# Kernel tuning notes

Measured on AMD Instinct MI355X. Metric: run time of the kernel, lower is better.

The kernel has to match this reference:

```python
import jax, jax.numpy as jnp
import numpy as np

H = 32          # num_attention_heads
HD = 128        # head_dim
HID = H * HD    # hidden_size = 4096
KB_LEN = 1024   # number of KB entries
TOPK = 128      # top_k_kb (dynamic_sparsify=True)
ROPE_THETA = 10000.0
PAD = -1000000000.0  # PADDING_VALUE


def rope_cos_sin(position_ids, head_dim, theta):
    inv_freq = 1.0 / (theta ** (jnp.arange(0, head_dim, 2, dtype=jnp.float32) / head_dim))
    freqs = position_ids.astype(jnp.float32)[..., None] * inv_freq  # [B,q,hd/2]
    emb = jnp.concatenate([freqs, freqs], axis=-1)                  # [B,q,hd]
    return jnp.cos(emb), jnp.sin(emb)


def rotate_half(x):
    half = x.shape[-1] // 2
    return jnp.concatenate([-x[..., half:], x[..., :half]], axis=-1)


def apply_rope(q, k, cos, sin):
    cos = cos[:, None]  # [B,1,q,hd]
    sin = sin[:, None]
    return q * cos + rotate_half(q) * sin, k * cos + rotate_half(k) * sin


def setup_inputs() -> dict:
    key = jax.random.key(0)
    ks = jax.random.split(key, 9)
    B, Q = 1, 2048
    w_scale = 0.02  # keep activations numerically sane
    hidden_states = jax.random.normal(ks[0], (B, Q, HID), jnp.float32)
    causal = jnp.where(jnp.tril(jnp.ones((Q, Q), bool)), 0.0, PAD).astype(jnp.float32)
    attention_mask = jnp.broadcast_to(causal[None, None], (B, 1, Q, Q))
    position_ids = jnp.broadcast_to(jnp.arange(Q)[None], (B, Q))
    kb_keys = jax.random.normal(ks[1], (KB_LEN, HID), jnp.float32)
    kb_values = jax.random.normal(ks[2], (KB_LEN, HID), jnp.float32)
    Wq = jax.random.normal(ks[3], (HID, HID), jnp.float32) * w_scale
    Wq2 = jax.random.normal(ks[4], (HID, HID), jnp.float32) * w_scale
    Wk = jax.random.normal(ks[5], (HID, HID), jnp.float32) * w_scale
    Wv = jax.random.normal(ks[6], (HID, HID), jnp.float32) * w_scale
    Wo = jax.random.normal(ks[7], (HID, HID), jnp.float32) * w_scale
    score_shift = jnp.zeros((H, 1), jnp.float32) - 3.0
    return {"hidden_states": hidden_states, "attention_mask": attention_mask,
            "position_ids": position_ids, "kb_keys": kb_keys, "kb_values": kb_values,
            "Wq": Wq, "Wq2": Wq2, "Wk": Wk, "Wv": Wv, "Wo": Wo,
            "score_shift": score_shift}


def kblam_attention(hidden_states, attention_mask, position_ids, kb_keys, kb_values,
                    Wq, Wq2, Wk, Wv, Wo, score_shift):
    B, Q, _ = hidden_states.shape
    scale = 1.0 / np.sqrt(HD)

    def heads(x):  # [B,Q,HID] -> [B,H,Q,HD]
        return x.reshape(B, Q, H, HD).transpose(0, 2, 1, 3)

    q = heads(hidden_states @ Wq.T)
    q2 = heads(hidden_states @ Wq2.T)   # second query head (used for KB top-k pruning)
    k = heads(hidden_states @ Wk.T)
    v = heads(hidden_states @ Wv.T)

    cos, sin = rope_cos_sin(position_ids, HD, ROPE_THETA)
    q, k = apply_rope(q, k, cos, sin)   # num_kv_groups == 1, repeat_kv is identity

    # --- KB path: [kb_len, H*HD] -> [B,H,kb_len,HD] ---
    kbk = jnp.broadcast_to(kb_keys.reshape(KB_LEN, H, HD).transpose(1, 0, 2)[None], (B, H, KB_LEN, HD))
    kbv = jnp.broadcast_to(kb_values.reshape(KB_LEN, H, HD).transpose(1, 0, 2)[None], (B, H, KB_LEN, HD))

    # prune_key_value (dynamic_sparsify): top-k KB rows by summed q2-scores
    aw2 = jnp.einsum('bhqd,bhkd->bhqk', q2, kbk) * scale          # [B,H,Q,KB_LEN]
    idx = jax.lax.stop_gradient(jax.lax.top_k(aw2.sum((1, 2)), TOPK)[1])  # [B,TOPK]
    gidx = jnp.broadcast_to(idx[:, None, :, None], (B, H, TOPK, HD))
    kbk = jnp.take_along_axis(kbk, gidx, axis=2)                  # [B,H,TOPK,HD]
    kbv = jnp.take_along_axis(kbv, gidx, axis=2)
    kb_len = TOPK

    k_all = jnp.concatenate([kbk, k], axis=2)                     # [B,H,kb_len+Q,HD]
    v_all = jnp.concatenate([kbv, v], axis=2)

    # kb attention mask: zeros, except fully-padded query rows get PADDING_VALUE
    padding_mask = jnp.all(attention_mask < 0, axis=-1, keepdims=True)  # [B,1,Q,1]
    kb_mask = jnp.where(padding_mask, PAD, 0.0).astype(attention_mask.dtype)
    mask = jnp.concatenate([jnp.broadcast_to(kb_mask, (B, 1, Q, kb_len)), attention_mask], axis=-1)

    attn = jnp.einsum('bhqd,bhkd->bhqk', q, k_all) * scale
    # learned per-head shift on KB scores (score_shift: [H,1], init -3)
    attn = attn.at[..., :kb_len].add(score_shift.reshape(1, H, 1, 1))
    attn = attn + mask
    attn = jax.nn.softmax(attn.astype(jnp.float32), axis=-1).astype(q.dtype)

    out = jnp.einsum('bhqk,bhkd->bhqd', attn, v_all)              # [B,H,Q,HD]
    out = out.transpose(0, 2, 1, 3).reshape(B, Q, HID)
    return out @ Wo.T


def reference(hidden_states, attention_mask, position_ids, kb_keys, kb_values,
              Wq, Wq2, Wk, Wv, Wo, score_shift):
    return kblam_attention(hidden_states, attention_mask, position_ids, kb_keys, kb_values,
                           Wq, Wq2, Wk, Wv, Wo, score_shift)
```

## Files before the change

kernel.cpp:

```cpp
#include <hip/hip_runtime.h>
#include <stdint.h>
#include <stddef.h>

#define NH 32
#define HD 128
#define HID 4096
#define QLEN 2048
#define KBLEN 1024
#define NTOPK 128
#define KVLEN 2176
#define PADV -1e9f
#define SCALE 0.08838834764831845f

typedef __attribute__((ext_vector_type(4))) float f32x4;
typedef __attribute__((ext_vector_type(4))) unsigned short u16x4;
typedef __attribute__((ext_vector_type(8))) short s16x8;
typedef __attribute__((ext_vector_type(4))) short s16x4;

typedef const __attribute__((address_space(1))) void* gas1_t;
typedef __attribute__((address_space(3))) void* las3_t;

__device__ __forceinline__ void gload_lds16(const void* g, void* l) {
  __builtin_amdgcn_global_load_lds((gas1_t)g, (las3_t)l, 16, 0, 0);
}

__device__ __forceinline__ unsigned short f2bf(float x) {
  union { float f; unsigned u; } z; z.f = x;
  unsigned r = z.u + 0x7fffu + ((z.u >> 16) & 1u);
  return (unsigned short)(r >> 16);
}

__device__ __forceinline__ s16x4 tr16(unsigned addr) {
  s16x4 r;
  asm volatile("ds_read_b64_tr_b16 %0, %1" : "=v"(r) : "v"(addr));
  return r;
}

__device__ __forceinline__ s16x8 cat8(s16x4 a, s16x4 b) {
  s16x8 r;
  r[0]=a[0]; r[1]=a[1]; r[2]=a[2]; r[3]=a[3];
  r[4]=b[0]; r[5]=b[1]; r[6]=b[2]; r[7]=b[3];
  return r;
}


__global__ void k_cast(const float* __restrict__ src, unsigned short* __restrict__ dst, int n4) {
  int i = blockIdx.x * 256 + threadIdx.x;
  if (i >= n4) return;
  f32x4 v = ((const f32x4*)src)[i];
  u16x4 o;
  o[0] = f2bf(v[0]); o[1] = f2bf(v[1]); o[2] = f2bf(v[2]); o[3] = f2bf(v[3]);
  ((u16x4*)dst)[i] = o;
}

__global__ void k_rowsum_p(const float* __restrict__ x, float* __restrict__ part) {
  int d = blockIdx.x * 256 + threadIdx.x;
  int q0 = blockIdx.y * 128;
  float acc = 0.f;
  for (int q = q0; q < q0 + 128; ++q) acc += x[(size_t)q * HID + d];
  part[(size_t)blockIdx.y * HID + d] = acc;
}
__global__ void k_rowsum_r(const float* __restrict__ part, float* __restrict__ out) {
  int d = blockIdx.x * 256 + threadIdx.x;
  float acc = 0.f;
#pragma unroll
  for (int i = 0; i < 16; ++i) acc += part[(size_t)i * HID + d];
  out[d] = acc;
}

__global__ void k_dotrows(const float* __restrict__ vec, const float* __restrict__ mat,
                          float* __restrict__ out, int K, float s) {
  int n = blockIdx.x * 4 + (threadIdx.x >> 6);
  int lane = threadIdx.x & 63;
  const float* row = mat + (size_t)n * K;
  float acc = 0.f;
  for (int j = lane; j < K; j += 64) acc += vec[j] * row[j];
#pragma unroll
  for (int off = 32; off > 0; off >>= 1) acc += __shfl_down(acc, off, 64);
  if (lane == 0) out[n] = acc * s;
}

__global__ void k_topk(const float* __restrict__ scores, int* __restrict__ idx) {
  __shared__ float s[KBLEN];
  int t = threadIdx.x;
  s[t] = scores[t];
  __syncthreads();
  float mine = s[t];
  int rank = 0;
  for (int j = 0; j < KBLEN; ++j) {
    float v = s[j];
    rank += (v > mine) || (v == mine && j < t);
  }
  if (rank < NTOPK) idx[rank] = t;
}

__global__ void k_cs(const int* __restrict__ pos_ids, float* __restrict__ cs) {
  int t = blockIdx.x * 256 + threadIdx.x;
  int p = t >> 6, i = t & 63;
  float pos = (float)pos_ids[p];
  float invf = powf(10000.0f, -(float)i / 64.0f);
  float a = pos * invf;
  cs[p * 128 + i] = cosf(a);
  cs[p * 128 + 64 + i] = sinf(a);
}

__global__ void k_rope(const float* __restrict__ raw, const float* __restrict__ cs,
                       unsigned short* __restrict__ dst, int RH, int RO) {
  int t = blockIdx.x * 256 + threadIdx.x;
  int i = t & 63;
  int hh = (t >> 6) & 31;
  int q = t >> 11;
  float x1 = raw[(size_t)q * HID + hh * HD + i];
  float x2 = raw[(size_t)q * HID + hh * HD + 64 + i];
  float c = cs[q * 128 + i];
  float sn = cs[q * 128 + 64 + i];
  size_t base = ((size_t)hh * RH + RO + q) * HD;
  dst[base + i]      = f2bf(x1 * c - x2 * sn);
  dst[base + 64 + i] = f2bf(x2 * c + x1 * sn);
}

__global__ void k_gather(const float* __restrict__ kbk, const float* __restrict__ kbv,
                         const int* __restrict__ idx,
                         unsigned short* __restrict__ kall, unsigned short* __restrict__ vall) {
  int t = blockIdx.x * 256 + threadIdx.x;
  int d = t & 127;
  int i = (t >> 7) & 127;
  int hh = t >> 14;
  int kr = idx[i];
  size_t src = (size_t)kr * HID + hh * HD + d;
  size_t dstoff = ((size_t)hh * KVLEN + i) * HD + d;
  kall[dstoff] = f2bf(kbk[src]);
  vall[dstoff] = f2bf(kbv[src]);
}

#define GBK 64
#define ABUF 8192
#define BBUF 16384
#define BUFE (ABUF + BBUF)

template<int MODE>
__global__ __launch_bounds__(512)
void gemm_bt(const unsigned short* __restrict__ A, const unsigned short* __restrict__ B,
             float* __restrict__ Cf, unsigned short* __restrict__ Cb,
             int M, int N, int K, int RH, int RO) {
  __shared__ unsigned short lds[3 * BUFE];
  const int tid = threadIdx.x;
  const int lane = tid & 63;
  const int wave = tid >> 6;
  const int lo = lane & 15, hi = lane >> 4;
  const int wm = wave >> 2, wn = wave & 3;

  const int nwg = gridDim.x * gridDim.y;
  const int orig = blockIdx.y * gridDim.x + blockIdx.x;
  const int wg = (orig & 7) * (nwg >> 3) + (orig >> 3);
  const int bx = wg % gridDim.x, by = wg / gridDim.x;
  const int m0 = by * 128, n0 = bx * 256;

  auto stageA = [&](int kt, int bufe, int g) {
    int j0 = g * 512 + wave * 64;
    int j = j0 + lane;
    int row = j >> 3, cb = j & 7;
    gload_lds16(A + (size_t)(m0 + row) * K + kt * GBK + ((cb ^ (row & 7)) << 3),
                (void*)(lds + bufe + j0 * 8));
  };
  auto stageB = [&](int kt, int bufe, int g) {
    int j0 = g * 512 + wave * 64;
    int j = j0 + lane;
    int row = j >> 3, cb = j & 7;
    gload_lds16(B + (size_t)(n0 + row) * K + kt * GBK + ((cb ^ (row & 7)) << 3),
                (void*)(lds + bufe + ABUF + j0 * 8));
  };

  f32x4 acc[4][4] = {};

  stageA(0, 0, 0); stageA(0, 0, 1);
  stageB(0, 0, 0); stageB(0, 0, 1); stageB(0, 0, 2); stageB(0, 0, 3);
  stageA(1, BUFE, 0); stageA(1, BUFE, 1);
  stageB(1, BUFE, 0); stageB(1, BUFE, 1); stageB(1, BUFE, 2); stageB(1, BUFE, 3);

  const int NT = K / GBK;
  const int sa = (lo & 7) << 3;
  int bi = 0;

  for (int kt = 0; kt < NT; ++kt) {
    if (kt < NT - 1) { asm volatile("s_waitcnt vmcnt(6)" ::: "memory"); }
    else             { asm volatile("s_waitcnt vmcnt(0)" ::: "memory"); }
    __builtin_amdgcn_sched_barrier(0);
    __builtin_amdgcn_s_barrier();
    __builtin_amdgcn_sched_barrier(0);

    const int bufe = bi * BUFE;
    const int nbufe = ((bi + 2 >= 3) ? bi - 1 : bi + 2) * BUFE;
    const bool pre = (kt + 2 < NT);
    const unsigned short* Ab = lds + bufe;
    const unsigned short* Bb = lds + bufe + ABUF;
    const int arow = wm * 64 + lo;
    const int brow = wn * 64 + lo;

    s16x8 af[4], b01[2], b23[2];
    const int c0 = (hi * 8) ^ sa;
    const int c1 = (32 + hi * 8) ^ sa;

#pragma unroll
    for (int i = 0; i < 4; ++i) af[i] = *(const s16x8*)(Ab + (arow + i * 16) * 64 + c0);
#pragma unroll
    for (int j = 0; j < 2; ++j) b01[j] = *(const s16x8*)(Bb + (brow + j * 16) * 64 + c0);
    if (pre) { stageA(kt + 2, nbufe, 0); stageA(kt + 2, nbufe, 1); }
    asm volatile("s_waitcnt lgkmcnt(0)" ::: "memory");
    __builtin_amdgcn_sched_barrier(0);
    __builtin_amdgcn_s_setprio(1);
#pragma unroll
    for (int i = 0; i < 4; ++i) {
      acc[i][0] = __builtin_amdgcn_mfma_f32_16x16x32_bf16(af[i], b01[0], acc[i][0], 0, 0, 0);
      acc[i][1] = __builtin_amdgcn_mfma_f32_16x16x32_bf16(af[i], b01[1], acc[i][1], 0, 0, 0);
    }
    __builtin_amdgcn_s_setprio(0);

#pragma unroll
    for (int j = 0; j < 2; ++j) b23[j] = *(const s16x8*)(Bb + (brow + (j + 2) * 16) * 64 + c0);
    if (pre) { stageB(kt + 2, nbufe, 0); stageB(kt + 2, nbufe, 1); }
    asm volatile("s_waitcnt lgkmcnt(0)" ::: "memory");
    __builtin_amdgcn_sched_barrier(0);
    __builtin_amdgcn_s_setprio(1);
#pragma unroll
    for (int i = 0; i < 4; ++i) {
      acc[i][2] = __builtin_amdgcn_mfma_f32_16x16x32_bf16(af[i], b23[0], acc[i][2], 0, 0, 0);
      acc[i][3] = __builtin_amdgcn_mfma_f32_16x16x32_bf16(af[i], b23[1], acc[i][3], 0, 0, 0);
    }
    __builtin_amdgcn_s_setprio(0);

#pragma unroll
    for (int i = 0; i < 4; ++i) af[i] = *(const s16x8*)(Ab + (arow + i * 16) * 64 + c1);
#pragma unroll
    for (int j = 0; j < 2; ++j) b01[j] = *(const s16x8*)(Bb + (brow + j * 16) * 64 + c1);
    if (pre) { stageB(kt + 2, nbufe, 2); stageB(kt + 2, nbufe, 3); }
    asm volatile("s_waitcnt lgkmcnt(0)" ::: "memory");
    __builtin_amdgcn_sched_barrier(0);
    __builtin_amdgcn_s_setprio(1);
#pragma unroll
    for (int i = 0; i < 4; ++i) {
      acc[i][0] = __builtin_amdgcn_mfma_f32_16x16x32_bf16(af[i], b01[0], acc[i][0], 0, 0, 0);
      acc[i][1] = __builtin_amdgcn_mfma_f32_16x16x32_bf16(af[i], b01[1], acc[i][1], 0, 0, 0);
    }
    __builtin_amdgcn_s_setprio(0);

#pragma unroll
    for (int j = 0; j < 2; ++j) b23[j] = *(const s16x8*)(Bb + (brow + (j + 2) * 16) * 64 + c1);
    asm volatile("s_waitcnt lgkmcnt(0)" ::: "memory");
    __builtin_amdgcn_sched_barrier(0);
    __builtin_amdgcn_s_setprio(1);
#pragma unroll
    for (int i = 0; i < 4; ++i) {
      acc[i][2] = __builtin_amdgcn_mfma_f32_16x16x32_bf16(af[i], b23[0], acc[i][2], 0, 0, 0);
      acc[i][3] = __builtin_amdgcn_mfma_f32_16x16x32_bf16(af[i], b23[1], acc[i][3], 0, 0, 0);
    }
    __builtin_amdgcn_s_setprio(0);

    bi = (bi + 1 == 3) ? 0 : bi + 1;
  }

#pragma unroll
  for (int i = 0; i < 4; ++i) {
#pragma unroll
    for (int j = 0; j < 4; ++j) {
#pragma unroll
      for (int r = 0; r < 4; ++r) {
        int row = m0 + wm * 64 + i * 16 + hi * 4 + r;
        int col = n0 + wn * 64 + j * 16 + lo;
        float v = acc[i][j][r];
        if (MODE == 0) {
          Cf[(size_t)row * N + col] = v;
        } else {
          int hh = col >> 7, d = col & 127;
          Cb[((size_t)hh * RH + RO + row) * HD + d] = f2bf(v);
        }
      }
    }
  }
}

__global__ __launch_bounds__(256)
void attn_kernel(const unsigned short* __restrict__ qh,
                 const unsigned short* __restrict__ kall,
                 const unsigned short* __restrict__ vall,
                 const float* __restrict__ sshift,
                 unsigned short* __restrict__ ctx) {
  __shared__ __align__(1024) unsigned short Ks[64 * 128];
  __shared__ __align__(1024) unsigned short Vs[64 * 128];
  __shared__ __align__(16)  unsigned short Plds[4][16 * 72];

  int orig = blockIdx.y * 16 + blockIdx.x;
  int wgid = (orig & 7) * 64 + (orig >> 3);
  int h = wgid >> 4;
  int xch = wgid & 15;

  const int tid = threadIdx.x;
  const int lane = tid & 63;
  const int wave = tid >> 6;
  const int lo = lane & 15;
  const int hi = lane >> 4;
  const float shift = sshift[h];

  const unsigned short* kb = kall + (size_t)h * KVLEN * HD;
  const unsigned short* vb = vall + (size_t)h * KVLEN * HD;

  const unsigned vsb = (unsigned)(uintptr_t)(&Vs[0]);

#pragma unroll 1
  for (int half = 0; half < 2; ++half) {
    const int qc = half ? (31 - xch) : xch;
    const int m0 = qc * 64;

    s16x8 qf[4];
    {
      const unsigned short* qp = qh + ((size_t)h * QLEN + m0 + wave * 16 + lo) * HD + hi * 8;
#pragma unroll
      for (int kc = 0; kc < 4; ++kc) qf[kc] = *(const s16x8*)(qp + kc * 32);
    }

    float m_run[4], l_run[4];
#pragma unroll
    for (int r = 0; r < 4; ++r) { m_run[r] = -1e30f; l_run[r] = 0.f; }
    f32x4 o[8] = {};

    const int nt = qc + 3;
    const int qrow = m0 + wave * 16 + hi * 4;

    for (int kt = 0; kt < nt; ++kt) {
      const unsigned short* kg = kb + (size_t)kt * 64 * HD;
      const unsigned short* vg = vb + (size_t)kt * 64 * HD;
      __syncthreads();
#pragma unroll
      for (int it = 0; it < 4; ++it) {
        int j0 = it * 256 + wave * 64;
        int j = j0 + lane;
        int row = j >> 4, cb = j & 15;
        gload_lds16(kg + row * 128 + ((cb ^ (row & 7)) * 8), (void*)(Ks + j0 * 8));
        int kq = j >> 6, dc = (j >> 3) & 7, kr = (j >> 1) & 3, hf = j & 1;
        gload_lds16(vg + (kq * 4 + kr) * 128 + dc * 16 + hf * 8, (void*)(Vs + j0 * 8));
      }
      __syncthreads();

      f32x4 s[4] = {};
#pragma unroll
      for (int kc = 0; kc < 4; ++kc) {
#pragma unroll
        for (int g = 0; g < 4; ++g) {
          int key = g * 16 + lo;
          s16x8 kf = *(const s16x8*)(Ks + key * 128 + (((kc * 4 + hi) ^ (key & 7)) * 8));
          s[g] = __builtin_amdgcn_mfma_f32_16x16x32_bf16(qf[kc], kf, s[g], 0, 0, 0);
        }
      }

      const int kvbase = kt * 64;
      float sv[4][4], mx[4];
#pragma unroll
      for (int r = 0; r < 4; ++r) {
        int qr = qrow + r;
#pragma unroll
        for (int g = 0; g < 4; ++g) {
          int kv = kvbase + g * 16 + lo;
          float v = s[g][r] * SCALE;
          v = (kv < NTOPK) ? (v + shift) : ((kv - NTOPK > qr) ? PADV : v);
          sv[g][r] = v;
        }
        mx[r] = fmaxf(fmaxf(sv[0][r], sv[1][r]), fmaxf(sv[2][r], sv[3][r]));
      }
#pragma unroll
      for (int off = 1; off < 16; off <<= 1)
#pragma unroll
        for (int r = 0; r < 4; ++r) mx[r] = fmaxf(mx[r], __shfl_xor(mx[r], off, 64));

      float alpha[4], rs[4];
#pragma unroll
      for (int r = 0; r < 4; ++r) {
        float mn = fmaxf(m_run[r], mx[r]);
        alpha[r] = __expf(m_run[r] - mn);
        m_run[r] = mn;
        float acc = 0.f;
#pragma unroll
        for (int g = 0; g < 4; ++g) {
          float p = __expf(sv[g][r] - mn);
          acc += p;
          Plds[wave][(hi * 4 + r) * 72 + g * 16 + lo] = f2bf(p);
        }
        rs[r] = acc;
      }
#pragma unroll
      for (int off = 1; off < 16; off <<= 1)
#pragma unroll
        for (int r = 0; r < 4; ++r) rs[r] += __shfl_xor(rs[r], off, 64);
#pragma unroll
      for (int r = 0; r < 4; ++r) l_run[r] = l_run[r] * alpha[r] + rs[r];
#pragma unroll
      for (int db = 0; db < 8; ++db)
#pragma unroll
        for (int r = 0; r < 4; ++r) o[db][r] *= alpha[r];

      s16x8 pf0 = *(const s16x8*)(&Plds[wave][lo * 72 + hi * 8]);
      s16x8 pf1 = *(const s16x8*)(&Plds[wave][lo * 72 + 32 + hi * 8]);
      const unsigned vb0 = vsb + hi * 2048 + lo * 8;
#pragma unroll
      for (int dbp = 0; dbp < 4; ++dbp) {
        s16x4 t[2][2][2];
#pragma unroll
        for (int dbi = 0; dbi < 2; ++dbi) {
          unsigned a0 = vb0 + (dbp * 2 + dbi) * 128;
          t[dbi][0][0] = tr16(a0);
          t[dbi][0][1] = tr16(a0 + 1024);
          t[dbi][1][0] = tr16(a0 + 8192);
          t[dbi][1][1] = tr16(a0 + 8192 + 1024);
        }
        asm volatile("s_waitcnt lgkmcnt(0)" ::: "memory");
        __builtin_amdgcn_sched_barrier(0);
#pragma unroll
        for (int dbi = 0; dbi < 2; ++dbi) {
          int db = dbp * 2 + dbi;
          o[db] = __builtin_amdgcn_mfma_f32_16x16x32_bf16(pf0, cat8(t[dbi][0][0], t[dbi][0][1]), o[db], 0, 0, 0);
          o[db] = __builtin_amdgcn_mfma_f32_16x16x32_bf16(pf1, cat8(t[dbi][1][0], t[dbi][1][1]), o[db], 0, 0, 0);
        }
      }
    }

#pragma unroll
    for (int db = 0; db < 8; ++db) {
#pragma unroll
      for (int r = 0; r < 4; ++r) {
        int row = qrow + r;
        int col = h * HD + db * 16 + lo;
        ctx[(size_t)row * HID + col] = f2bf(o[db][r] / l_run[r]);
      }
    }
  }
}


extern "C" void kernel_launch(void* const* d_in, const int* in_sizes, int n_in,
                              void* d_out, int out_size, void* d_ws, size_t ws_size,
                              hipStream_t stream) {
  const float* hidden    = (const float*)d_in[0];
  const int*   pos       = (const int*)d_in[2];
  const float* kb_keys   = (const float*)d_in[3];
  const float* kb_values = (const float*)d_in[4];
  const float* Wq        = (const float*)d_in[5];
  const float* Wq2       = (const float*)d_in[6];
  const float* Wk        = (const float*)d_in[7];
  const float* Wv        = (const float*)d_in[8];
  const float* Wo        = (const float*)d_in[9];
  const float* sshift    = (const float*)d_in[10];
  float* out = (float*)d_out;

  char* ws = (char*)d_ws;
  size_t off = 0;
  auto alloc = [&](size_t bytes) { char* p = ws + off; off += (bytes + 255) & ~(size_t)255; return p; };
  unsigned short* hidden_bf = (unsigned short*)alloc((size_t)QLEN * HID * 2);
  unsigned short* wbuf      = (unsigned short*)alloc((size_t)HID * HID * 2);
  float*          qraw      = (float*)alloc((size_t)QLEN * HID * 4);
  float*          kraw      = (float*)alloc((size_t)QLEN * HID * 4);
  unsigned short* qbf       = (unsigned short*)alloc((size_t)NH * QLEN * HD * 2);
  unsigned short* kallp     = (unsigned short*)alloc((size_t)NH * KVLEN * HD * 2);
  unsigned short* vallp     = (unsigned short*)alloc((size_t)NH * KVLEN * HD * 2);
  unsigned short* ctx       = (unsigned short*)alloc((size_t)QLEN * HID * 2);
  float*          cs        = (float*)alloc((size_t)QLEN * 128 * 4);
  float*          part      = (float*)alloc((size_t)16 * HID * 4);
  float*          hsum      = (float*)alloc(HID * 4);
  float*          qs        = (float*)alloc(HID * 4);
  float*          scores    = (float*)alloc(KBLEN * 4);
  int*            idx       = (int*)alloc(NTOPK * 4);

  dim3 blk(256);

  k_cast<<<QLEN * HID / 4 / 256, blk, 0, stream>>>(hidden, hidden_bf, QLEN * HID / 4);
  k_rowsum_p<<<dim3(HID / 256, 16), blk, 0, stream>>>(hidden, part);
  k_rowsum_r<<<HID / 256, blk, 0, stream>>>(part, hsum);
  k_dotrows<<<HID / 4, blk, 0, stream>>>(hsum, Wq2, qs, HID, 1.0f);
  k_dotrows<<<KBLEN / 4, blk, 0, stream>>>(qs, kb_keys, scores, HID, SCALE);
  k_topk<<<1, KBLEN, 0, stream>>>(scores, idx);
  k_cs<<<QLEN * 64 / 256, blk, 0, stream>>>(pos, cs);

  dim3 ggrid(HID / 256, QLEN / 128);
  dim3 gblk(512);
  int wcast_blocks = HID * HID / 4 / 256;

  k_cast<<<wcast_blocks, blk, 0, stream>>>(Wq, wbuf, HID * HID / 4);
  gemm_bt<0><<<ggrid, gblk, 0, stream>>>(hidden_bf, wbuf, qraw, nullptr, QLEN, HID, HID, 0, 0);
  k_cast<<<wcast_blocks, blk, 0, stream>>>(Wk, wbuf, HID * HID / 4);
  gemm_bt<0><<<ggrid, gblk, 0, stream>>>(hidden_bf, wbuf, kraw, nullptr, QLEN, HID, HID, 0, 0);
  k_cast<<<wcast_blocks, blk, 0, stream>>>(Wv, wbuf, HID * HID / 4);
  gemm_bt<1><<<ggrid, gblk, 0, stream>>>(hidden_bf, wbuf, nullptr, vallp, QLEN, HID, HID, KVLEN, NTOPK);

  k_rope<<<QLEN * NH * 64 / 256, blk, 0, stream>>>(qraw, cs, qbf, QLEN, 0);
  k_rope<<<QLEN * NH * 64 / 256, blk, 0, stream>>>(kraw, cs, kallp, KVLEN, NTOPK);

  k_gather<<<NH * NTOPK * HD / 256, blk, 0, stream>>>(kb_keys, kb_values, idx, kallp, vallp);

  dim3 agrid(16, NH);
  attn_kernel<<<agrid, blk, 0, stream>>>(qbf, kallp, vallp, sshift, ctx);

  k_cast<<<wcast_blocks, blk, 0, stream>>>(Wo, wbuf, HID * HID / 4);
  gemm_bt<0><<<ggrid, gblk, 0, stream>>>(ctx, wbuf, out, nullptr, QLEN, HID, HID, 0, 0);
}
```

Baseline: 595.6 us.

## Fuse RoPE into QK GEMM epilogue, double-buffer attention KV, defer softmax rescale

The Q and K projection GEMMs now apply RoPE in their epilogue. The wave-to-column mapping is changed so each wave holds both halves (d and d+64) of a head, and bf16 is written directly. This removes the fp32 qraw/kraw round trips and the two separate rope kernels. The attention kernel double-buffers K/V tiles in LDS so the next tile loads during compute. It also switches to exp2 with log2e-prescaled scores and skips the running-max rescale unless the max grows by more than a threshold. That adds LDS use and a small risk of overflow-related precision drift.

```diff
diff --git a/kernel.cpp b/kernel.cpp
--- a/kernel.cpp
+++ b/kernel.cpp
@@ -11,6 +11,9 @@
 #define KVLEN 2176
 #define PADV -1e9f
 #define SCALE 0.08838834764831845f
+#define LOG2E 1.4426950408889634f
+#define SC2 (SCALE * LOG2E)
+#define DEFER_THR 8.0f
 
 typedef __attribute__((ext_vector_type(4))) float f32x4;
 typedef __attribute__((ext_vector_type(4))) unsigned short u16x4;
@@ -94,29 +97,13 @@
   if (rank < NTOPK) idx[rank] = t;
 }
 
-__global__ void k_cs(const int* __restrict__ pos_ids, float* __restrict__ cs) {
+__global__ void k_cs(const int* __restrict__ pos_ids, float2* __restrict__ cs) {
   int t = blockIdx.x * 256 + threadIdx.x;
   int p = t >> 6, i = t & 63;
   float pos = (float)pos_ids[p];
   float invf = powf(10000.0f, -(float)i / 64.0f);
   float a = pos * invf;
-  cs[p * 128 + i] = cosf(a);
-  cs[p * 128 + 64 + i] = sinf(a);
-}
-
-__global__ void k_rope(const float* __restrict__ raw, const float* __restrict__ cs,
-                       unsigned short* __restrict__ dst, int RH, int RO) {
-  int t = blockIdx.x * 256 + threadIdx.x;
-  int i = t & 63;
-  int hh = (t >> 6) & 31;
-  int q = t >> 11;
-  float x1 = raw[(size_t)q * HID + hh * HD + i];
-  float x2 = raw[(size_t)q * HID + hh * HD + 64 + i];
-  float c = cs[q * 128 + i];
-  float sn = cs[q * 128 + 64 + i];
-  size_t base = ((size_t)hh * RH + RO + q) * HD;
-  dst[base + i]      = f2bf(x1 * c - x2 * sn);
-  dst[base + 64 + i] = f2bf(x2 * c + x1 * sn);
+  cs[p * 64 + i] = make_float2(cosf(a), sinf(a));
 }
 
 __global__ void k_gather(const float* __restrict__ kbk, const float* __restrict__ kbv,
@@ -142,7 +129,7 @@
 __global__ __launch_bounds__(512)
 void gemm_bt(const unsigned short* __restrict__ A, const unsigned short* __restrict__ B,
              float* __restrict__ Cf, unsigned short* __restrict__ Cb,
-             int M, int N, int K, int RH, int RO) {
+             int M, int N, int K, int RH, int RO, const float2* __restrict__ cs2) {
   __shared__ unsigned short lds[3 * BUFE];
   const int tid = threadIdx.x;
   const int lane = tid & 63;
@@ -180,6 +167,7 @@
 
   const int NT = K / GBK;
   const int sa = (lo & 7) << 3;
+  const int bbase = (wn >> 1) * 128 + (wn & 1) * 32;
   int bi = 0;
 
   for (int kt = 0; kt < NT; ++kt) {
@@ -195,7 +183,7 @@
     const unsigned short* Ab = lds + bufe;
     const unsigned short* Bb = lds + bufe + ABUF;
     const int arow = wm * 64 + lo;
-    const int brow = wn * 64 + lo;
+    const int brow = bbase + lo;
 
     s16x8 af[4], b01[2], b23[2];
     const int c0 = (hi * 8) ^ sa;
@@ -203,8 +191,8 @@
 
 #pragma unroll
     for (int i = 0; i < 4; ++i) af[i] = *(const s16x8*)(Ab + (arow + i * 16) * 64 + c0);
-#pragma unroll
-    for (int j = 0; j < 2; ++j) b01[j] = *(const s16x8*)(Bb + (brow + j * 16) * 64 + c0);
+    b01[0] = *(const s16x8*)(Bb + (brow +  0) * 64 + c0);
+    b01[1] = *(const s16x8*)(Bb + (brow + 16) * 64 + c0);
     if (pre) { stageA(kt + 2, nbufe, 0); stageA(kt + 2, nbufe, 1); }
     asm volatile("s_waitcnt lgkmcnt(0)" ::: "memory");
     __builtin_amdgcn_sched_barrier(0);
@@ -216,8 +204,8 @@
     }
     __builtin_amdgcn_s_setprio(0);
 
-#pragma unroll
-    for (int j = 0; j < 2; ++j) b23[j] = *(const s16x8*)(Bb + (brow + (j + 2) * 16) * 64 + c0);
+    b23[0] = *(const s16x8*)(Bb + (brow + 64) * 64 + c0);
+    b23[1] = *(const s16x8*)(Bb + (brow + 80) * 64 + c0);
     if (pre) { stageB(kt + 2, nbufe, 0); stageB(kt + 2, nbufe, 1); }
     asm volatile("s_waitcnt lgkmcnt(0)" ::: "memory");
     __builtin_amdgcn_sched_barrier(0);
@@ -231,8 +219,8 @@
 
 #pragma unroll
     for (int i = 0; i < 4; ++i) af[i] = *(const s16x8*)(Ab + (arow + i * 16) * 64 + c1);
-#pragma unroll
-    for (int j = 0; j < 2; ++j) b01[j] = *(const s16x8*)(Bb + (brow + j * 16) * 64 + c1);
+    b01[0] = *(const s16x8*)(Bb + (brow +  0) * 64 + c1);
+    b01[1] = *(const s16x8*)(Bb + (brow + 16) * 64 + c1);
     if (pre) { stageB(kt + 2, nbufe, 2); stageB(kt + 2, nbufe, 3); }
     asm volatile("s_waitcnt lgkmcnt(0)" ::: "memory");
     __builtin_amdgcn_sched_barrier(0);
@@ -244,8 +232,8 @@
     }
     __builtin_amdgcn_s_setprio(0);
 
-#pragma unroll
-    for (int j = 0; j < 2; ++j) b23[j] = *(const s16x8*)(Bb + (brow + (j + 2) * 16) * 64 + c1);
+    b23[0] = *(const s16x8*)(Bb + (brow + 64) * 64 + c1);
+    b23[1] = *(const s16x8*)(Bb + (brow + 80) * 64 + c1);
     asm volatile("s_waitcnt lgkmcnt(0)" ::: "memory");
     __builtin_amdgcn_sched_barrier(0);
     __builtin_amdgcn_s_setprio(1);
@@ -259,20 +247,40 @@
     bi = (bi + 1 == 3) ? 0 : bi + 1;
   }
 
-#pragma unroll
-  for (int i = 0; i < 4; ++i) {
-#pragma unroll
-    for (int j = 0; j < 4; ++j) {
-#pragma unroll
-      for (int r = 0; r < 4; ++r) {
-        int row = m0 + wm * 64 + i * 16 + hi * 4 + r;
-        int col = n0 + wn * 64 + j * 16 + lo;
-        float v = acc[i][j][r];
-        if (MODE == 0) {
-          Cf[(size_t)row * N + col] = v;
-        } else {
+  if (MODE == 2) {
+#pragma unroll
+    for (int i = 0; i < 4; ++i) {
+#pragma unroll
+      for (int j = 0; j < 2; ++j) {
+#pragma unroll
+        for (int r = 0; r < 4; ++r) {
+          int row = m0 + wm * 64 + i * 16 + hi * 4 + r;
+          int col = n0 + bbase + j * 16 + lo;
           int hh = col >> 7, d = col & 127;
-          Cb[((size_t)hh * RH + RO + row) * HD + d] = f2bf(v);
+          float2 cp = cs2[row * 64 + d];
+          float x1 = acc[i][j][r], x2 = acc[i][j + 2][r];
+          size_t base = ((size_t)hh * RH + RO + row) * HD;
+          Cb[base + d]      = f2bf(x1 * cp.x - x2 * cp.y);
+          Cb[base + d + 64] = f2bf(x2 * cp.x + x1 * cp.y);
+        }
+      }
+    }
+  } else {
+#pragma unroll
+    for (int i = 0; i < 4; ++i) {
+#pragma unroll
+      for (int j = 0; j < 4; ++j) {
+#pragma unroll
+        for (int r = 0; r < 4; ++r) {
+          int row = m0 + wm * 64 + i * 16 + hi * 4 + r;
+          int col = n0 + bbase + (j >> 1) * 64 + (j & 1) * 16 + lo;
+          float v = acc[i][j][r];
+          if (MODE == 0) {
+            Cf[(size_t)row * N + col] = v;
+          } else {
+            int hh = col >> 7, d = col & 127;
+            Cb[((size_t)hh * RH + RO + row) * HD + d] = f2bf(v);
+          }
         }
       }
     }
@@ -285,8 +293,8 @@
                  const unsigned short* __restrict__ vall,
                  const float* __restrict__ sshift,
                  unsigned short* __restrict__ ctx) {
-  __shared__ __align__(1024) unsigned short Ks[64 * 128];
-  __shared__ __align__(1024) unsigned short Vs[64 * 128];
+  __shared__ __align__(1024) unsigned short Ks[2][64 * 128];
+  __shared__ __align__(1024) unsigned short Vs[2][64 * 128];
   __shared__ __align__(16)  unsigned short Plds[4][16 * 72];
 
   int orig = blockIdx.y * 16 + blockIdx.x;
@@ -299,12 +307,10 @@
   const int wave = tid >> 6;
   const int lo = lane & 15;
   const int hi = lane >> 4;
-  const float shift = sshift[h];
+  const float shiftL = sshift[h] * LOG2E;
 
   const unsigned short* kb = kall + (size_t)h * KVLEN * HD;
   const unsigned short* vb = vall + (size_t)h * KVLEN * HD;
-
-  const unsigned vsb = (unsigned)(uintptr_t)(&Vs[0]);
 
 #pragma unroll 1
   for (int half = 0; half < 2; ++half) {
@@ -325,21 +331,27 @@
 
     const int nt = qc + 3;
     const int qrow = m0 + wave * 16 + hi * 4;
-
-    for (int kt = 0; kt < nt; ++kt) {
+    int buf = 0;
+
+    auto STAGE = [&](int kt, int b) {
       const unsigned short* kg = kb + (size_t)kt * 64 * HD;
       const unsigned short* vg = vb + (size_t)kt * 64 * HD;
-      __syncthreads();
 #pragma unroll
       for (int it = 0; it < 4; ++it) {
         int j0 = it * 256 + wave * 64;
         int j = j0 + lane;
         int row = j >> 4, cb = j & 15;
-        gload_lds16(kg + row * 128 + ((cb ^ (row & 7)) * 8), (void*)(Ks + j0 * 8));
+        gload_lds16(kg + row * 128 + ((cb ^ (row & 7)) * 8), (void*)(Ks[b] + j0 * 8));
         int kq = j >> 6, dc = (j >> 3) & 7, kr = (j >> 1) & 3, hf = j & 1;
-        gload_lds16(vg + (kq * 4 + kr) * 128 + dc * 16 + hf * 8, (void*)(Vs + j0 * 8));
-      }
-      __syncthreads();
+        gload_lds16(vg + (kq * 4 + kr) * 128 + dc * 16 + hf * 8, (void*)(Vs[b] + j0 * 8));
+      }
+    };
+
+    STAGE(0, 0);
+    __syncthreads();
+
+    for (int kt = 0; kt < nt; ++kt) {
+      if (kt + 1 < nt) STAGE(kt + 1, buf ^ 1);
 
       f32x4 s[4] = {};
 #pragma unroll
@@ -347,7 +359,7 @@
 #pragma unroll
         for (int g = 0; g < 4; ++g) {
           int key = g * 16 + lo;
-          s16x8 kf = *(const s16x8*)(Ks + key * 128 + (((kc * 4 + hi) ^ (key & 7)) * 8));
+          s16x8 kf = *(const s16x8*)(Ks[buf] + key * 128 + (((kc * 4 + hi) ^ (key & 7)) * 8));
           s[g] = __builtin_amdgcn_mfma_f32_16x16x32_bf16(qf[kc], kf, s[g], 0, 0, 0);
         }
       }
@@ -360,8 +372,8 @@
 #pragma unroll
         for (int g = 0; g < 4; ++g) {
           int kv = kvbase + g * 16 + lo;
-          float v = s[g][r] * SCALE;
-          v = (kv < NTOPK) ? (v + shift) : ((kv - NTOPK > qr) ? PADV : v);
+          float v = s[g][r] * SC2;
+          v = (kv < NTOPK) ? (v + shiftL) : ((kv - NTOPK > qr) ? PADV : v);
           sv[g][r] = v;
         }
         mx[r] = fmaxf(fmaxf(sv[0][r], sv[1][r]), fmaxf(sv[2][r], sv[3][r]));
@@ -371,16 +383,28 @@
 #pragma unroll
         for (int r = 0; r < 4; ++r) mx[r] = fmaxf(mx[r], __shfl_xor(mx[r], off, 64));
 
-      float alpha[4], rs[4];
+      bool need = false;
+#pragma unroll
+      for (int r = 0; r < 4; ++r) need = need || (mx[r] > m_run[r] + DEFER_THR);
+      if (need) {
+#pragma unroll
+        for (int r = 0; r < 4; ++r) {
+          float mn = fmaxf(m_run[r], mx[r]);
+          float alpha = __builtin_amdgcn_exp2f(m_run[r] - mn);
+          m_run[r] = mn;
+          l_run[r] *= alpha;
+#pragma unroll
+          for (int db = 0; db < 8; ++db) o[db][r] *= alpha;
+        }
+      }
+
+      float rs[4];
 #pragma unroll
       for (int r = 0; r < 4; ++r) {
-        float mn = fmaxf(m_run[r], mx[r]);
-        alpha[r] = __expf(m_run[r] - mn);
-        m_run[r] = mn;
         float acc = 0.f;
 #pragma unroll
         for (int g = 0; g < 4; ++g) {
-          float p = __expf(sv[g][r] - mn);
+          float p = __builtin_amdgcn_exp2f(sv[g][r] - m_run[r]);
           acc += p;
           Plds[wave][(hi * 4 + r) * 72 + g * 16 + lo] = f2bf(p);
         }
@@ -391,15 +415,11 @@
 #pragma unroll
         for (int r = 0; r < 4; ++r) rs[r] += __shfl_xor(rs[r], off, 64);
 #pragma unroll
-      for (int r = 0; r < 4; ++r) l_run[r] = l_run[r] * alpha[r] + rs[r];
-#pragma unroll
-      for (int db = 0; db < 8; ++db)
-#pragma unroll
-        for (int r = 0; r < 4; ++r) o[db][r] *= alpha[r];
+      for (int r = 0; r < 4; ++r) l_run[r] += rs[r];
 
       s16x8 pf0 = *(const s16x8*)(&Plds[wave][lo * 72 + hi * 8]);
       s16x8 pf1 = *(const s16x8*)(&Plds[wave][lo * 72 + 32 + hi * 8]);
-      const unsigned vb0 = vsb + hi * 2048 + lo * 8;
+      const unsigned vb0 = (unsigned)(uintptr_t)(&Vs[buf][0]) + hi * 2048 + lo * 8;
 #pragma unroll
       for (int dbp = 0; dbp < 4; ++dbp) {
         s16x4 t[2][2][2];
@@ -420,6 +440,9 @@
           o[db] = __builtin_amdgcn_mfma_f32_16x16x32_bf16(pf1, cat8(t[dbi][1][0], t[dbi][1][1]), o[db], 0, 0, 0);
         }
       }
+
+      __syncthreads();
+      buf ^= 1;
     }
 
 #pragma unroll
@@ -455,13 +478,11 @@
   auto alloc = [&](size_t bytes) { char* p = ws + off; off += (bytes + 255) & ~(size_t)255; return p; };
   unsigned short* hidden_bf = (unsigned short*)alloc((size_t)QLEN * HID * 2);
   unsigned short* wbuf      = (unsigned short*)alloc((size_t)HID * HID * 2);
-  float*          qraw      = (float*)alloc((size_t)QLEN * HID * 4);
-  float*          kraw      = (float*)alloc((size_t)QLEN * HID * 4);
   unsigned short* qbf       = (unsigned short*)alloc((size_t)NH * QLEN * HD * 2);
   unsigned short* kallp     = (unsigned short*)alloc((size_t)NH * KVLEN * HD * 2);
   unsigned short* vallp     = (unsigned short*)alloc((size_t)NH * KVLEN * HD * 2);
   unsigned short* ctx       = (unsigned short*)alloc((size_t)QLEN * HID * 2);
-  float*          cs        = (float*)alloc((size_t)QLEN * 128 * 4);
+  float2*         cs2       = (float2*)alloc((size_t)QLEN * 64 * 8);
   float*          part      = (float*)alloc((size_t)16 * HID * 4);
   float*          hsum      = (float*)alloc(HID * 4);
   float*          qs        = (float*)alloc(HID * 4);
@@ -476,21 +497,18 @@
   k_dotrows<<<HID / 4, blk, 0, stream>>>(hsum, Wq2, qs, HID, 1.0f);
   k_dotrows<<<KBLEN / 4, blk, 0, stream>>>(qs, kb_keys, scores, HID, SCALE);
   k_topk<<<1, KBLEN, 0, stream>>>(scores, idx);
-  k_cs<<<QLEN * 64 / 256, blk, 0, stream>>>(pos, cs);
+  k_cs<<<QLEN * 64 / 256, blk, 0, stream>>>(pos, cs2);
 
   dim3 ggrid(HID / 256, QLEN / 128);
   dim3 gblk(512);
   int wcast_blocks = HID * HID / 4 / 256;
 
   k_cast<<<wcast_blocks, blk, 0, stream>>>(Wq, wbuf, HID * HID / 4);
-  gemm_bt<0><<<ggrid, gblk, 0, stream>>>(hidden_bf, wbuf, qraw, nullptr, QLEN, HID, HID, 0, 0);
+  gemm_bt<2><<<ggrid, gblk, 0, stream>>>(hidden_bf, wbuf, nullptr, qbf, QLEN, HID, HID, QLEN, 0, cs2);
   k_cast<<<wcast_blocks, blk, 0, stream>>>(Wk, wbuf, HID * HID / 4);
-  gemm_bt<0><<<ggrid, gblk, 0, stream>>>(hidden_bf, wbuf, kraw, nullptr, QLEN, HID, HID, 0, 0);
+  gemm_bt<2><<<ggrid, gblk, 0, stream>>>(hidden_bf, wbuf, nullptr, kallp, QLEN, HID, HID, KVLEN, NTOPK, cs2);
   k_cast<<<wcast_blocks, blk, 0, stream>>>(Wv, wbuf, HID * HID / 4);
-  gemm_bt<1><<<ggrid, gblk, 0, stream>>>(hidden_bf, wbuf, nullptr, vallp, QLEN, HID, HID, KVLEN, NTOPK);
-
-  k_rope<<<QLEN * NH * 64 / 256, blk, 0, stream>>>(qraw, cs, qbf, QLEN, 0);
-  k_rope<<<QLEN * NH * 64 / 256, blk, 0, stream>>>(kraw, cs, kallp, KVLEN, NTOPK);
+  gemm_bt<1><<<ggrid, gblk, 0, stream>>>(hidden_bf, wbuf, nullptr, vallp, QLEN, HID, HID, KVLEN, NTOPK, cs2);
 
   k_gather<<<NH * NTOPK * HD / 256, blk, 0, stream>>>(kb_keys, kb_values, idx, kallp, vallp);
 
@@ -498,5 +516,5 @@
   attn_kernel<<<agrid, blk, 0, stream>>>(qbf, kallp, vallp, sshift, ctx);
 
   k_cast<<<wcast_blocks, blk, 0, stream>>>(Wo, wbuf, HID * HID / 4);
-  gemm_bt<0><<<ggrid, gblk, 0, stream>>>(ctx, wbuf, out, nullptr, QLEN, HID, HID, 0, 0);
-}
+  gemm_bt<0><<<ggrid, gblk, 0, stream>>>(ctx, wbuf, out, nullptr, QLEN, HID, HID, 0, 0, cs2);
+}
```

After: 577.2 us. -3.1%, faster.
